# Kernel optimization log

Hardware: AMD Instinct MI355X
Metric: run time of the kernel (lower is better)

Reference implementation:

```python
import jax, jax.numpy as jnp
import numpy as np

B, H, W, C = 4, 256, 256, 32
K = 5  # per-pixel kernel spatial size (K*K = 25 taps)


def setup_inputs() -> dict:
    key = jax.random.key(0)
    k1, k2, k3 = jax.random.split(key, 3)
    feat = jax.random.normal(k1, (B, H, W, C), dtype=jnp.float32)
    kernel = jax.random.normal(k2, (B, H, W, K * K), dtype=jnp.float32)
    bias = jax.random.normal(k3, (C,), dtype=jnp.float32)
    return {"feat": feat, "kernel": kernel, "bias": bias}


def reference(feat, kernel, bias):
    # Per-pixel predicted convolution (kernel prediction network style):
    # out[b,h,w,c] = sum_{i,j} feat[b, h+i-p, w+j-p, c] * kernel[b,h,w, i*K+j]
    # Kernel taps are shared across channels; SAME zero padding.
    b, h, w, c = feat.shape
    kk = kernel.shape[-1]
    k = int(round(np.sqrt(kk)))
    pad = k // 2
    fp = jnp.pad(feat, ((0, 0), (pad, pad), (pad, pad), (0, 0)))
    out = jnp.zeros_like(feat)
    for i in range(k):          # small fixed K*K loop; avoids materializing
        for j in range(k):      # the [B,H,W,K*K,C] patch tensor
            tap = kernel[..., i * k + j][..., None]          # [B,H,W,1]
            out = out + fp[:, i:i + h, j:j + w, :] * tap      # [B,H,W,C]
    return out + bias  # tf.nn.bias_add, channels_last
```

## Files before the change

kernel.cpp:

```cpp
#include <hip/hip_runtime.h>


#define BB 4
#define HH 256
#define WW 256
#define CC 32
#define KK 5
#define VH 4
#define TW 32
#define TPB 256

__global__ __launch_bounds__(TPB) void kpn_conv_kernel(
    const float* __restrict__ feat,
    const float* __restrict__ kern,
    const float* __restrict__ bias,
    float* __restrict__ out)
{
    __shared__ float sk[VH * TW * KK * KK];

    const int t = threadIdx.x;

    const int bw = blockIdx.x & 7;
    const int bh = (blockIdx.x >> 3) & 63;
    const int b  = blockIdx.x >> 9;
    const int h0 = bh * VH;
    const int w0 = bw * TW;

    const float* kb = kern + ((size_t)((b * HH + h0) * WW + w0)) * (KK * KK);
    #pragma unroll
    for (int it = 0; it < 4; ++it) {
        int idx = t + it * TPB;
        if (idx < VH * TW * KK * KK / 4) {
            int row = idx / 200;
            int off = (idx - row * 200) * 4;
            *(float4*)(sk + row * (TW * KK * KK) + off) =
                *(const float4*)(kb + (size_t)row * WW * KK * KK + off);
        }
    }
    __syncthreads();

    const int cg = (t & 7) * 4;
    const int wL = t >> 3;
    const int w  = w0 + wL;

    const float4 bz = *(const float4*)(bias + cg);
    float4 acc[VH];
    #pragma unroll
    for (int oh = 0; oh < VH; ++oh) acc[oh] = bz;

    const float* fb = feat + (((size_t)b) << 16) * CC;

    #pragma unroll
    for (int r = 0; r < VH + KK - 1; ++r) {
        const int hh = h0 + r - (KK / 2);
        if ((unsigned)hh < (unsigned)HH) {
            float4 f[KK];
            #pragma unroll
            for (int j = 0; j < KK; ++j) {
                int ww  = w + j - (KK / 2);
                int wwc = min(max(ww, 0), WW - 1);
                f[j] = *(const float4*)(fb + ((((size_t)hh << 8) + wwc) << 5) + cg);
            }
            #pragma unroll
            for (int j = 0; j < KK; ++j) {
                int ww = w + j - (KK / 2);
                if ((unsigned)ww >= (unsigned)WW) {
                    f[j].x = 0.f; f[j].y = 0.f; f[j].z = 0.f; f[j].w = 0.f;
                }
            }
            #pragma unroll
            for (int oh = 0; oh < VH; ++oh) {
                const int ii = r - oh;
                if (ii >= 0 && ii < KK) {
                    const float* wp = sk + oh * (TW * KK * KK) + wL * (KK * KK) + ii * KK;
                    #pragma unroll
                    for (int j = 0; j < KK; ++j) {
                        const float wg = wp[j];
                        acc[oh].x += f[j].x * wg;
                        acc[oh].y += f[j].y * wg;
                        acc[oh].z += f[j].z * wg;
                        acc[oh].w += f[j].w * wg;
                    }
                }
            }
        }
    }

    #pragma unroll
    for (int oh = 0; oh < VH; ++oh) {
        const size_t pix = (size_t)(b * HH + h0 + oh) * WW + w;
        *(float4*)(out + pix * CC + cg) = acc[oh];
    }
}

extern "C" void kernel_launch(void* const* d_in, const int* in_sizes, int n_in,
                              void* d_out, int out_size, void* d_ws, size_t ws_size,
                              hipStream_t stream) {
    const float* feat = (const float*)d_in[0];
    const float* kern = (const float*)d_in[1];
    const float* bias = (const float*)d_in[2];
    float* out = (float*)d_out;

    dim3 grid(BB * (HH / VH) * (WW / TW));
    dim3 block(TPB);
    kpn_conv_kernel<<<grid, block, 0, stream>>>(feat, kern, bias, out);
}
```

Before: 117.2 us.

## Shrink row tile, pre-mask taps in LDS, and double-buffer feature rows

Cuts the rows per block from 4 to 2, doubling the grid, and raises the occupancy hint with launch_bounds(256,6). Kernel taps are reordered in shared memory into padded 8-wide rows with the out-of-bounds taps zeroed in advance, so the feature loads can use clamped addresses with no per-element masking. Feature rows are software-prefetched one row ahead so loads overlap the FMAs. The trade-off is less vertical reuse of feature rows: each block reads 6 rows for 2 outputs instead of 8 rows for 4, which raises feature traffic through L2.

```diff
diff --git a/kernel.cpp b/kernel.cpp
--- a/kernel.cpp
+++ b/kernel.cpp
@@ -6,35 +6,41 @@
 #define WW 256
 #define CC 32
 #define KK 5
-#define VH 4
+#define OHR 2
 #define TW 32
 #define TPB 256
 
-__global__ __launch_bounds__(TPB) void kpn_conv_kernel(
+__global__ __launch_bounds__(TPB, 6) void kpn_conv_kernel(
     const float* __restrict__ feat,
     const float* __restrict__ kern,
     const float* __restrict__ bias,
     float* __restrict__ out)
 {
-    __shared__ float sk[VH * TW * KK * KK];
+    __shared__ float sk[OHR * KK * TW * 8];
 
-    const int t = threadIdx.x;
-
+    const int t  = threadIdx.x;
     const int bw = blockIdx.x & 7;
-    const int bh = (blockIdx.x >> 3) & 63;
-    const int b  = blockIdx.x >> 9;
-    const int h0 = bh * VH;
+    const int bh = (blockIdx.x >> 3) & 127;
+    const int b  = blockIdx.x >> 10;
+    const int h0 = bh * OHR;
     const int w0 = bw * TW;
 
-    const float* kb = kern + ((size_t)((b * HH + h0) * WW + w0)) * (KK * KK);
+    const float* kb = kern + (size_t)((b * HH + h0) * WW + w0) * (KK * KK);
     #pragma unroll
-    for (int it = 0; it < 4; ++it) {
+    for (int it = 0; it < 7; ++it) {
         int idx = t + it * TPB;
-        if (idx < VH * TW * KK * KK / 4) {
-            int row = idx / 200;
-            int off = (idx - row * 200) * 4;
-            *(float4*)(sk + row * (TW * KK * KK) + off) =
-                *(const float4*)(kb + (size_t)row * WW * KK * KK + off);
+        if (idx < OHR * TW * KK * KK) {
+            int oh  = idx / (TW * KK * KK);
+            int rem = idx - oh * (TW * KK * KK);
+            int wl  = rem / (KK * KK);
+            int tap = rem - wl * (KK * KK);
+            int i   = tap / KK;
+            int j   = tap - i * KK;
+            int hh  = h0 + oh + i - (KK / 2);
+            int ww  = w0 + wl + j - (KK / 2);
+            bool v  = ((unsigned)hh < (unsigned)HH) && ((unsigned)ww < (unsigned)WW);
+            float val = kb[oh * (WW * KK * KK) + rem];
+            sk[((oh * KK + i) * TW + wl) * 8 + j] = v ? val : 0.0f;
         }
     }
     __syncthreads();
@@ -44,50 +50,57 @@
     const int w  = w0 + wL;
 
     const float4 bz = *(const float4*)(bias + cg);
-    float4 acc[VH];
+    float4 acc[OHR];
     #pragma unroll
-    for (int oh = 0; oh < VH; ++oh) acc[oh] = bz;
+    for (int oh = 0; oh < OHR; ++oh) acc[oh] = bz;
 
     const float* fb = feat + (((size_t)b) << 16) * CC;
 
+    int wc[KK];
     #pragma unroll
-    for (int r = 0; r < VH + KK - 1; ++r) {
-        const int hh = h0 + r - (KK / 2);
-        if ((unsigned)hh < (unsigned)HH) {
-            float4 f[KK];
-            #pragma unroll
-            for (int j = 0; j < KK; ++j) {
-                int ww  = w + j - (KK / 2);
-                int wwc = min(max(ww, 0), WW - 1);
-                f[j] = *(const float4*)(fb + ((((size_t)hh << 8) + wwc) << 5) + cg);
-            }
-            #pragma unroll
-            for (int j = 0; j < KK; ++j) {
-                int ww = w + j - (KK / 2);
-                if ((unsigned)ww >= (unsigned)WW) {
-                    f[j].x = 0.f; f[j].y = 0.f; f[j].z = 0.f; f[j].w = 0.f;
-                }
-            }
-            #pragma unroll
-            for (int oh = 0; oh < VH; ++oh) {
-                const int ii = r - oh;
-                if (ii >= 0 && ii < KK) {
-                    const float* wp = sk + oh * (TW * KK * KK) + wL * (KK * KK) + ii * KK;
-                    #pragma unroll
-                    for (int j = 0; j < KK; ++j) {
-                        const float wg = wp[j];
-                        acc[oh].x += f[j].x * wg;
-                        acc[oh].y += f[j].y * wg;
-                        acc[oh].z += f[j].z * wg;
-                        acc[oh].w += f[j].w * wg;
-                    }
-                }
-            }
-        }
+    for (int j = 0; j < KK; ++j) wc[j] = min(max(w + j - (KK / 2), 0), WW - 1);
+
+    float4 cur[KK], nxt[KK];
+    {
+        const int hh = min(max(h0 - (KK / 2), 0), HH - 1);
+        const float* rp = fb + (((size_t)hh) << 13);
+        #pragma unroll
+        for (int j = 0; j < KK; ++j)
+            cur[j] = *(const float4*)(rp + (wc[j] << 5) + cg);
     }
 
     #pragma unroll
-    for (int oh = 0; oh < VH; ++oh) {
+    for (int r = 0; r < OHR + KK - 1; ++r) {
+        if (r < OHR + KK - 2) {
+            const int hh = min(max(h0 + r + 1 - (KK / 2), 0), HH - 1);
+            const float* rp = fb + (((size_t)hh) << 13);
+            #pragma unroll
+            for (int j = 0; j < KK; ++j)
+                nxt[j] = *(const float4*)(rp + (wc[j] << 5) + cg);
+        }
+        #pragma unroll
+        for (int oh = 0; oh < OHR; ++oh) {
+            const int i = r - oh;
+            if (i >= 0 && i < KK) {
+                const float* wp = sk + ((oh * KK + i) * TW + wL) * 8;
+                const float4 w4 = *(const float4*)wp;
+                const float  w5 = wp[4];
+                acc[oh].x += cur[0].x * w4.x + cur[1].x * w4.y + cur[2].x * w4.z
+                           + cur[3].x * w4.w + cur[4].x * w5;
+                acc[oh].y += cur[0].y * w4.x + cur[1].y * w4.y + cur[2].y * w4.z
+                           + cur[3].y * w4.w + cur[4].y * w5;
+                acc[oh].z += cur[0].z * w4.x + cur[1].z * w4.y + cur[2].z * w4.z
+                           + cur[3].z * w4.w + cur[4].z * w5;
+                acc[oh].w += cur[0].w * w4.x + cur[1].w * w4.y + cur[2].w * w4.z
+                           + cur[3].w * w4.w + cur[4].w * w5;
+            }
+        }
+        #pragma unroll
+        for (int j = 0; j < KK; ++j) cur[j] = nxt[j];
+    }
+
+    #pragma unroll
+    for (int oh = 0; oh < OHR; ++oh) {
         const size_t pix = (size_t)(b * HH + h0 + oh) * WW + w;
         *(float4*)(out + pix * CC + cg) = acc[oh];
     }
@@ -101,7 +114,7 @@
     const float* bias = (const float*)d_in[2];
     float* out = (float*)d_out;
 
-    dim3 grid(BB * (HH / VH) * (WW / TW));
+    dim3 grid(BB * (HH / OHR) * (WW / TW));
     dim3 block(TPB);
     kpn_conv_kernel<<<grid, block, 0, stream>>>(feat, kern, bias, out);
 }
```

Result: slower. 138.2 us (+17.8%).

## Fold zero-padding into LDS kernel taps and transpose tap layout

Applied to the files above, without the earlier changes.

The per-pixel kernel taps are staged into shared memory transposed to a [oh][i][j][w] layout. Taps whose source pixel falls outside the image are zeroed at staging time, so the main loop can clamp feature coordinates and load unconditionally with no row branch or column masking. The scalar staging loop replaces float4 global loads with per-element index math and divisions. __launch_bounds__ is removed, which may change register allocation.

```diff
diff --git a/kernel.cpp b/kernel.cpp
--- a/kernel.cpp
+++ b/kernel.cpp
@@ -10,32 +10,34 @@
 #define TW 32
 #define TPB 256
 
-__global__ __launch_bounds__(TPB) void kpn_conv_kernel(
+__global__ void kpn_conv_kernel(
     const float* __restrict__ feat,
     const float* __restrict__ kern,
     const float* __restrict__ bias,
     float* __restrict__ out)
 {
-    __shared__ float sk[VH * TW * KK * KK];
+    __shared__ float sk[VH * KK * KK * TW];
 
-    const int t = threadIdx.x;
-
+    const int t  = threadIdx.x;
     const int bw = blockIdx.x & 7;
     const int bh = (blockIdx.x >> 3) & 63;
     const int b  = blockIdx.x >> 9;
     const int h0 = bh * VH;
     const int w0 = bw * TW;
 
-    const float* kb = kern + ((size_t)((b * HH + h0) * WW + w0)) * (KK * KK);
-    #pragma unroll
-    for (int it = 0; it < 4; ++it) {
-        int idx = t + it * TPB;
-        if (idx < VH * TW * KK * KK / 4) {
-            int row = idx / 200;
-            int off = (idx - row * 200) * 4;
-            *(float4*)(sk + row * (TW * KK * KK) + off) =
-                *(const float4*)(kb + (size_t)row * WW * KK * KK + off);
-        }
+    const float* kb = kern + (size_t)((b * HH + h0) * WW + w0) * (KK * KK);
+    for (int idx = t; idx < VH * TW * KK * KK; idx += TPB) {
+        int oh  = idx / (TW * KK * KK);
+        int rem = idx - oh * (TW * KK * KK);
+        int wl  = rem / (KK * KK);
+        int tap = rem - wl * (KK * KK);
+        int i   = tap / KK;
+        int j   = tap - i * KK;
+        int hh  = h0 + oh + i - (KK / 2);
+        int ww  = w0 + wl + j - (KK / 2);
+        bool v  = ((unsigned)hh < (unsigned)HH) && ((unsigned)ww < (unsigned)WW);
+        float val = kb[(size_t)oh * WW * (KK * KK) + rem];
+        sk[((oh * KK + i) * KK + j) * TW + wl] = v ? val : 0.0f;
     }
     __syncthreads();
 
@@ -50,37 +52,32 @@
 
     const float* fb = feat + (((size_t)b) << 16) * CC;
 
+    int wc[KK];
+    #pragma unroll
+    for (int j = 0; j < KK; ++j) wc[j] = min(max(w + j - (KK / 2), 0), WW - 1);
+
     #pragma unroll
     for (int r = 0; r < VH + KK - 1; ++r) {
-        const int hh = h0 + r - (KK / 2);
-        if ((unsigned)hh < (unsigned)HH) {
-            float4 f[KK];
-            #pragma unroll
-            for (int j = 0; j < KK; ++j) {
-                int ww  = w + j - (KK / 2);
-                int wwc = min(max(ww, 0), WW - 1);
-                f[j] = *(const float4*)(fb + ((((size_t)hh << 8) + wwc) << 5) + cg);
-            }
-            #pragma unroll
-            for (int j = 0; j < KK; ++j) {
-                int ww = w + j - (KK / 2);
-                if ((unsigned)ww >= (unsigned)WW) {
-                    f[j].x = 0.f; f[j].y = 0.f; f[j].z = 0.f; f[j].w = 0.f;
-                }
-            }
-            #pragma unroll
-            for (int oh = 0; oh < VH; ++oh) {
-                const int ii = r - oh;
-                if (ii >= 0 && ii < KK) {
-                    const float* wp = sk + oh * (TW * KK * KK) + wL * (KK * KK) + ii * KK;
-                    #pragma unroll
-                    for (int j = 0; j < KK; ++j) {
-                        const float wg = wp[j];
-                        acc[oh].x += f[j].x * wg;
-                        acc[oh].y += f[j].y * wg;
-                        acc[oh].z += f[j].z * wg;
-                        acc[oh].w += f[j].w * wg;
-                    }
+        const int hh = min(max(h0 + r - (KK / 2), 0), HH - 1);
+        const float* rp = fb + (((size_t)hh) << 13);
+
+        float4 f[KK];
+        #pragma unroll
+        for (int j = 0; j < KK; ++j)
+            f[j] = *(const float4*)(rp + (wc[j] << 5) + cg);
+
+        #pragma unroll
+        for (int oh = 0; oh < VH; ++oh) {
+            const int i = r - oh;
+            if (i >= 0 && i < KK) {
+                const float* wp = sk + ((oh * KK + i) * KK) * TW + wL;
+                #pragma unroll
+                for (int j = 0; j < KK; ++j) {
+                    const float wg = wp[j * TW];
+                    acc[oh].x += f[j].x * wg;
+                    acc[oh].y += f[j].y * wg;
+                    acc[oh].z += f[j].z * wg;
+                    acc[oh].w += f[j].w * wg;
                 }
             }
         }
```

New measurement: 132.7 us. 1.13x slower.
